# Kernel optimization log

Hardware: AMD Instinct MI355X
Metric: run time of the kernel (lower is better)

The kernel has to match this reference:

```python
import jax, jax.numpy as jnp
import numpy as np

B, L, DK, DV = 16, 8192, 128, 128
ALPHA, LR, BETA = 0.02, 0.1, 0.9
SCALE = 0.05  # keeps lr*||k||^2 small -> stable delta-rule recurrence


def setup_inputs() -> dict:
    key = jax.random.key(0)
    kq, kk, kv = jax.random.split(key, 3)
    Q = jax.random.normal(kq, (B, L, DK), dtype=jnp.float32) * SCALE
    K = jax.random.normal(kk, (B, L, DK), dtype=jnp.float32) * SCALE
    V = jax.random.normal(kv, (B, L, DV), dtype=jnp.float32) * SCALE
    return {"Q": Q, "K": K, "V": V}


def reference(Q, K, V):
    # TitansMemory: reset -> per-step update_step(k_t, v_t) -> read(q_t).
    # W_t = (1-alpha) W_{t-1} - lr * m_t,  m_t = beta m_{t-1} + (1-beta) grad_t
    # grad_t = 2 (W_{t-1} k_t - v_t) k_t^T ;  y_t = W_t q_t
    b, l, dk = K.shape
    dv = V.shape[-1]
    W0 = jnp.zeros((b, dv, dk), dtype=K.dtype)
    m0 = jnp.zeros_like(W0)

    def step(carry, inp):
        W, m = carry
        k, v, q = inp  # [B,dk], [B,dv], [B,dk]
        resid = jnp.einsum('bvk,bk->bv', W, k) - v          # Wk - v
        grad = 2.0 * resid[:, :, None] * k[:, None, :]       # [B,dv,dk]
        m = BETA * m + (1.0 - BETA) * grad
        W = (1.0 - ALPHA) * W - LR * m
        y = jnp.einsum('bvk,bk->bv', W, q)                   # read with updated W
        return (W, m), y

    xs = (jnp.swapaxes(K, 0, 1), jnp.swapaxes(V, 0, 1), jnp.swapaxes(Q, 0, 1))
    (_, _), Y = jax.lax.scan(step, (W0, m0), xs)             # Y: [L,B,dv]
    return jnp.swapaxes(Y, 0, 1)                              # [B,L,dv]
```

## Files before the change

### kernel.cpp

```cpp
#include <hip/hip_runtime.h>


#define L_ 8192
#define D_ 128

typedef __attribute__((ext_vector_type(4))) float f4;
typedef __attribute__((ext_vector_type(2))) float f2;
typedef __attribute__((ext_vector_type(2))) unsigned int u2;

constexpr float A_    = 0.98f;
constexpr float BETA_ = 0.9f;
constexpr float C_S   = -0.02f;

template <int CTRL>
__device__ __forceinline__ float dpp_add(float x) {
  int y = __builtin_amdgcn_update_dpp(0, __float_as_int(x), CTRL, 0xF, 0xF, true);
  return x + __int_as_float(y);
}

__device__ __forceinline__ float half_sum_all(float x) {
  x = dpp_add<0x121>(x);
  x = dpp_add<0x122>(x);
  x = dpp_add<0x124>(x);
  x = dpp_add<0x128>(x);
  u2 p = __builtin_amdgcn_permlane16_swap(__float_as_uint(x), __float_as_uint(x),
                                          false, false);
  return __uint_as_float(p.x) + __uint_as_float(p.y);
}

#define GLD4(dst, addr, OFF) \
  asm volatile("global_load_dwordx4 %0, %1, off offset:" OFF : "=v"(dst) : "v"(addr))
#define GLD1(dst, addr, OFF) \
  asm volatile("global_load_dword %0, %1, off offset:" OFF : "=v"(dst) : "v"(addr))

#define ISSUE_CHUNK(kb, qb, vb)                            \
  do {                                                     \
    GLD4(kb[0], ka64, "0");    GLD4(qb[0], qa64, "0");    GLD1(vb[0], va64, "0");    \
    GLD4(kb[1], ka64, "512");  GLD4(qb[1], qa64, "512");  GLD1(vb[1], va64, "512");  \
    GLD4(kb[2], ka64, "1024"); GLD4(qb[2], qa64, "1024"); GLD1(vb[2], va64, "1024"); \
    GLD4(kb[3], ka64, "1536"); GLD4(qb[3], qa64, "1536"); GLD1(vb[3], va64, "1536"); \
    GLD4(kb[4], ka64, "2048"); GLD4(qb[4], qa64, "2048"); GLD1(vb[4], va64, "2048"); \
    GLD4(kb[5], ka64, "2560"); GLD4(qb[5], qa64, "2560"); GLD1(vb[5], va64, "2560"); \
    GLD4(kb[6], ka64, "3072"); GLD4(qb[6], qa64, "3072"); GLD1(vb[6], va64, "3072"); \
    GLD4(kb[7], ka64, "3584"); GLD4(qb[7], qa64, "3584"); GLD1(vb[7], va64, "3584"); \
    uint64_t bump_ = (sc < 1023) ? 4096u : 0u;             \
    ka64 += bump_; qa64 += bump_; va64 += bump_; ++sc;     \
  } while (0)

#define WAITP                                              \
  do {                                                     \
    asm volatile("s_waitcnt vmcnt(24)");                   \
    __builtin_amdgcn_sched_barrier(0);                     \
  } while (0)

__global__ __launch_bounds__(64, 1)
void TitansMemory_188978561365_kernel(const float* __restrict__ Q,
                                      const float* __restrict__ K,
                                      const float* __restrict__ V,
                                      float* __restrict__ Y) {
  const int lane  = threadIdx.x;
  const int wid   = blockIdx.x;
  const int batch = wid >> 6;
  const int col   = (lane & 31) << 2;

  const size_t bbase = (size_t)batch * (size_t)L_ * D_;
  uint64_t ka64 = (uint64_t)(K + bbase + col);
  uint64_t qa64 = (uint64_t)(Q + bbase + col);
  uint64_t va64 = (uint64_t)(V + bbase + ((wid & 63) << 1) + (lane >> 5));
  float* yb = Y + bbase + ((wid & 63) << 1) + (lane >> 5)
                + (size_t)((lane >> 4) & 1) * D_;
  int sc = 0;

  const f4 av = {A_, A_, A_, A_};
  const f4 bv = {BETA_, BETA_, BETA_, BETA_};

  f4 w = {0.f, 0.f, 0.f, 0.f}, m = {0.f, 0.f, 0.f, 0.f};

  f4 kA[8], qA[8]; float vA[8];
  f4 kB[8], qB[8]; float vB[8];
  float ey[8];

  auto step = [&](const f4& k, const f4& q, float v) -> float {
    f4 d = w * k;
    f2 dp = {d.x + d.z, d.y + d.w};
    float dot = half_sum_all(dp.x + dp.y);
    float s = fmaf(C_S, dot, (-C_S) * v);
    f4 s4 = {s, s, s, s};
    m = __builtin_elementwise_fma(s4, k, bv * m);
    w = __builtin_elementwise_fma(av, w, m);
    f4 e = w * q;
    f2 ep = {e.x + e.z, e.y + e.w};
    return ep.x + ep.y;
  };

  auto flushY = [&]() {
#pragma unroll
    for (int p = 0; p < 4; ++p) {
      u2 r = __builtin_amdgcn_permlane16_swap(__float_as_uint(ey[2 * p]),
                                              __float_as_uint(ey[2 * p + 1]),
                                              false, false);
      float c = __uint_as_float(r.x) + __uint_as_float(r.y);
      c = dpp_add<0x121>(c);
      c = dpp_add<0x122>(c);
      c = dpp_add<0x124>(c);
      c = dpp_add<0x128>(c);
      if ((lane & 15) == 0) yb[(size_t)(2 * p) * D_] = c;
    }
    yb += 8 * D_;
  };

  ISSUE_CHUNK(kA, qA, vA);
  ISSUE_CHUNK(kB, qB, vB);

  for (int it = 0; it < L_ / 32; ++it) {
    WAITP;
#pragma unroll
    for (int j = 0; j < 8; ++j) ey[j] = step(kA[j], qA[j], vA[j]);
    flushY();
    ISSUE_CHUNK(kA, qA, vA);
    WAITP;
#pragma unroll
    for (int j = 0; j < 8; ++j) ey[j] = step(kB[j], qB[j], vB[j]);
    flushY();
    ISSUE_CHUNK(kB, qB, vB);
    WAITP;
#pragma unroll
    for (int j = 0; j < 8; ++j) ey[j] = step(kA[j], qA[j], vA[j]);
    flushY();
    ISSUE_CHUNK(kA, qA, vA);
    WAITP;
#pragma unroll
    for (int j = 0; j < 8; ++j) ey[j] = step(kB[j], qB[j], vB[j]);
    flushY();
    ISSUE_CHUNK(kB, qB, vB);
  }
}

extern "C" void kernel_launch(void* const* d_in, const int* in_sizes, int n_in,
                              void* d_out, int out_size, void* d_ws, size_t ws_size,
                              hipStream_t stream) {
  const float* Q = (const float*)d_in[0];
  const float* K = (const float*)d_in[1];
  const float* V = (const float*)d_in[2];
  float* Y = (float*)d_out;
  dim3 grid(1024), block(64);
  hipLaunchKernelGGL(TitansMemory_188978561365_kernel, grid, block, 0, stream,
                     Q, K, V, Y);
}
```

Baseline: 1.190 ms.

## Break serial dot-product reduction chain via algebraic lookahead within 8-step windows

Rewrites each step's scalar s_t = c·(W_{t-1}k_t) - c·v_t so that most of it is computed off the critical path. W_{t-1}k_t is expanded as A·(W_{t-2}k_t) + β·(m_{t-2}k_t) + s_{t-1}(k_{t-1}·k_t). The cross-lane reductions for k_{t-1}·k_t and for the base terms are batched two at a time and issued ahead of the step that needs them, so the serial dependency becomes a single FMA on s per step. This adds extra reductions and dot products per step and slightly changes floating-point association. Loop structure is unchanged: 512 iterations of two 8-step windows, the same 8192 steps as before.

```diff
diff --git a/kernel.cpp b/kernel.cpp
--- a/kernel.cpp
+++ b/kernel.cpp
@@ -11,6 +11,9 @@
 constexpr float A_    = 0.98f;
 constexpr float BETA_ = 0.9f;
 constexpr float C_S   = -0.02f;
+constexpr float CA_   = C_S * A_;
+constexpr float CB_   = C_S * BETA_;
+constexpr float CV_   = -C_S;
 
 template <int CTRL>
 __device__ __forceinline__ float dpp_add(float x) {
@@ -18,14 +21,26 @@
   return x + __int_as_float(y);
 }
 
-__device__ __forceinline__ float half_sum_all(float x) {
-  x = dpp_add<0x121>(x);
-  x = dpp_add<0x122>(x);
-  x = dpp_add<0x124>(x);
-  x = dpp_add<0x128>(x);
-  u2 p = __builtin_amdgcn_permlane16_swap(__float_as_uint(x), __float_as_uint(x),
+__device__ __forceinline__ float fold4(f4 d) {
+  f2 t = {d.x + d.z, d.y + d.w};
+  return t.x + t.y;
+}
+
+__device__ __forceinline__ u2 swap16(float a, float b) {
+  return __builtin_amdgcn_permlane16_swap(__float_as_uint(a), __float_as_uint(b),
                                           false, false);
-  return __uint_as_float(p.x) + __uint_as_float(p.y);
+}
+
+__device__ __forceinline__ f2 reduce2(float a, float b) {
+  u2 r = swap16(a, b);
+  float c = __uint_as_float(r.x) + __uint_as_float(r.y);
+  c = dpp_add<0x121>(c);
+  c = dpp_add<0x122>(c);
+  c = dpp_add<0x124>(c);
+  c = dpp_add<0x128>(c);
+  u2 u = swap16(c, c);
+  return {__uint_as_float(u.x),
+          __uint_as_float(u.y)};
 }
 
 #define GLD4(dst, addr, OFF) \
@@ -75,30 +90,57 @@
   const f4 bv = {BETA_, BETA_, BETA_, BETA_};
 
   f4 w = {0.f, 0.f, 0.f, 0.f}, m = {0.f, 0.f, 0.f, 0.f};
+  float ey[8];
 
   f4 kA[8], qA[8]; float vA[8];
   f4 kB[8], qB[8]; float vB[8];
-  float ey[8];
 
-  auto step = [&](const f4& k, const f4& q, float v) -> float {
-    f4 d = w * k;
-    f2 dp = {d.x + d.z, d.y + d.w};
-    float dot = half_sum_all(dp.x + dp.y);
-    float s = fmaf(C_S, dot, (-C_S) * v);
+  auto apply = [&](float s, const f4& kj, const f4& qj, float& eyj) {
     f4 s4 = {s, s, s, s};
-    m = __builtin_elementwise_fma(s4, k, bv * m);
+    m = __builtin_elementwise_fma(s4, kj, bv * m);
     w = __builtin_elementwise_fma(av, w, m);
-    f4 e = w * q;
-    f2 ep = {e.x + e.z, e.y + e.w};
-    return ep.x + ep.y;
+    eyj = fold4(w * qj);
   };
 
-  auto flushY = [&]() {
+  auto mkbase = [&](const f4& kp2, float vp2) -> float {
+    f2 P = reduce2(fold4(w * kp2), fold4(m * kp2));
+    return fmaf(CA_, P.x, fmaf(CB_, P.y, CV_ * vp2));
+  };
+
+  auto window = [&](f4 (&kX)[8], f4 (&qX)[8], float (&vX)[8]) {
+    f2 h0  = reduce2(fold4(w * kX[0]), fold4(w * kX[1]));
+    f2 h1  = reduce2(fold4(m * kX[1]), fold4(kX[0] * kX[1]));
+    f2 g23 = reduce2(fold4(kX[1] * kX[2]), fold4(kX[2] * kX[3]));
+    f2 g45 = reduce2(fold4(kX[3] * kX[4]), fold4(kX[4] * kX[5]));
+    f2 g67 = reduce2(fold4(kX[5] * kX[6]), fold4(kX[6] * kX[7]));
+
+    float s = fmaf(C_S, h0.x, CV_ * vX[0]);
+    apply(s, kX[0], qX[0], ey[0]);
+    float b2 = mkbase(kX[2], vX[2]);
+    float base1 = fmaf(CA_, h0.y, fmaf(CB_, h1.x, CV_ * vX[1]));
+    s = fmaf(s, C_S * h1.y, base1);
+    apply(s, kX[1], qX[1], ey[1]);
+    float b3 = mkbase(kX[3], vX[3]);
+    s = fmaf(s, C_S * g23.x, b2);
+    apply(s, kX[2], qX[2], ey[2]);
+    float b4 = mkbase(kX[4], vX[4]);
+    s = fmaf(s, C_S * g23.y, b3);
+    apply(s, kX[3], qX[3], ey[3]);
+    float b5 = mkbase(kX[5], vX[5]);
+    s = fmaf(s, C_S * g45.x, b4);
+    apply(s, kX[4], qX[4], ey[4]);
+    float b6 = mkbase(kX[6], vX[6]);
+    s = fmaf(s, C_S * g45.y, b5);
+    apply(s, kX[5], qX[5], ey[5]);
+    float b7 = mkbase(kX[7], vX[7]);
+    s = fmaf(s, C_S * g67.x, b6);
+    apply(s, kX[6], qX[6], ey[6]);
+    s = fmaf(s, C_S * g67.y, b7);
+    apply(s, kX[7], qX[7], ey[7]);
+
 #pragma unroll
     for (int p = 0; p < 4; ++p) {
-      u2 r = __builtin_amdgcn_permlane16_swap(__float_as_uint(ey[2 * p]),
-                                              __float_as_uint(ey[2 * p + 1]),
-                                              false, false);
+      u2 r = swap16(ey[2 * p], ey[2 * p + 1]);
       float c = __uint_as_float(r.x) + __uint_as_float(r.y);
       c = dpp_add<0x121>(c);
       c = dpp_add<0x122>(c);
@@ -107,32 +149,17 @@
       if ((lane & 15) == 0) yb[(size_t)(2 * p) * D_] = c;
     }
     yb += 8 * D_;
+    ISSUE_CHUNK(kX, qX, vX);
   };
 
   ISSUE_CHUNK(kA, qA, vA);
   ISSUE_CHUNK(kB, qB, vB);
 
-  for (int it = 0; it < L_ / 32; ++it) {
+  for (int it = 0; it < 512; ++it) {
     WAITP;
-#pragma unroll
-    for (int j = 0; j < 8; ++j) ey[j] = step(kA[j], qA[j], vA[j]);
-    flushY();
-    ISSUE_CHUNK(kA, qA, vA);
+    window(kA, qA, vA);
     WAITP;
-#pragma unroll
-    for (int j = 0; j < 8; ++j) ey[j] = step(kB[j], qB[j], vB[j]);
-    flushY();
-    ISSUE_CHUNK(kB, qB, vB);
-    WAITP;
-#pragma unroll
-    for (int j = 0; j < 8; ++j) ey[j] = step(kA[j], qA[j], vA[j]);
-    flushY();
-    ISSUE_CHUNK(kA, qA, vA);
-    WAITP;
-#pragma unroll
-    for (int j = 0; j < 8; ++j) ey[j] = step(kB[j], qB[j], vB[j]);
-    flushY();
-    ISSUE_CHUNK(kB, qB, vB);
+    window(kB, qB, vB);
   }
 }
 
```

After: 1.294 ms. +8.7%, slower.
